# Performance work log

Hardware: AMD Instinct MI355X
Metric: run time of the kernel (lower is better)

## Reference

```python
import jax, jax.numpy as jnp
import numpy as np

B, S, D = 1, 2048, 2048
H, G = 32, 8            # n_heads, n_groups
HPG = H // G            # heads per group = 4
HD = D // H             # head_dim = 64


def setup_inputs() -> dict:
    key = jax.random.key(0)
    ks = jax.random.split(key, 5)
    w_scale = 0.02
    return {
        "x":  jax.random.normal(ks[0], (B, S, D), dtype=jnp.float32),
        "Wq": jax.random.normal(ks[1], (D, D), dtype=jnp.float32) * w_scale,
        "bq": jnp.zeros((D,), dtype=jnp.float32),
        "Wk": jax.random.normal(ks[2], (G * HD, D), dtype=jnp.float32) * w_scale,
        "bk": jnp.zeros((G * HD,), dtype=jnp.float32),
        "Wv": jax.random.normal(ks[3], (G * HD, D), dtype=jnp.float32) * w_scale,
        "bv": jnp.zeros((G * HD,), dtype=jnp.float32),
        "Wo": jax.random.normal(ks[4], (D, D), dtype=jnp.float32) * w_scale,
        "bo": jnp.zeros((D,), dtype=jnp.float32),
    }


def reference(x, Wq, bq, Wk, bk, Wv, bv, Wo, bo):
    b, n, _ = x.shape
    # projections (torch Linear: y = x @ W.T + b)
    q = x @ Wq.T + bq                              # [b, n, D]
    k = x @ Wk.T + bk                              # [b, n, G*HD]
    v = x @ Wv.T + bv                              # [b, n, G*HD]
    # q: [b, n, H, HD] -> [b, H, n, HD] -> split heads as (g h): [b, G, HPG, n, HD]
    q = q.reshape(b, n, H, HD).transpose(0, 2, 1, 3).reshape(b, G, HPG, n, HD)
    k = k.reshape(b, n, G, HD).transpose(0, 2, 1, 3)   # [b, G, n, HD]
    v = v.reshape(b, n, G, HD).transpose(0, 2, 1, 3)   # [b, G, n, HD]
    scale = 1.0 / jnp.sqrt(jnp.asarray(HD, dtype=q.dtype))
    attn_score = jnp.einsum('bghnd,bgsd->bghns', q, k) * scale
    attn_prob = jax.nn.softmax(attn_score, axis=-1)
    out = jnp.einsum('bghns,bgsd->bghnd', attn_prob, v)   # [b, G, HPG, n, HD]
    # faithful to original: rearrange 'b g h n d -> b n (h g d)' (h-major, g-minor)
    out = out.transpose(0, 3, 2, 1, 4).reshape(b, n, HPG * G * HD)
    return out @ Wo.T + bo
```

## Files before the change

### kernel.cpp

```cpp
#include <hip/hip_runtime.h>
#include <hip/hip_bf16.h>

constexpr int kS   = 2048;
constexpr int kD   = 2048;
constexpr int kG   = 8;
constexpr int kHD  = 64;
constexpr int kGHD = 512;
constexpr int kNQKV = kD + 2 * kGHD;

constexpr float kQScale = 0.125f * 1.4426950408889634f;

typedef __attribute__((ext_vector_type(8)))  _Float16 f16x8;
typedef __attribute__((ext_vector_type(4)))  float    f32x4;
typedef __attribute__((ext_vector_type(16))) float    f32x16;
typedef __attribute__((ext_vector_type(4)))  unsigned int u32x4;

__device__ __forceinline__ ushort f2h(float x) {
    return __builtin_bit_cast(ushort, (_Float16)x);
}
__device__ __forceinline__ float fast_exp2(float x) {
    return __builtin_amdgcn_exp2f(x);
}
__device__ __forceinline__ unsigned int pkrtz(float a, float b) {
    auto r = __builtin_amdgcn_cvt_pkrtz(a, b);
    return __builtin_bit_cast(unsigned int, r);
}

__global__ __launch_bounds__(256) void cvt_all(
    const float* __restrict__ x,  const float* __restrict__ Wq,
    const float* __restrict__ Wk, const float* __restrict__ Wv,
    const float* __restrict__ Wo, const float* __restrict__ bq,
    const float* __restrict__ bk, const float* __restrict__ bv,
    ushort* __restrict__ xf, ushort* __restrict__ wqkvf,
    ushort* __restrict__ wof, float* __restrict__ bqkv)
{
    constexpr size_t Nx  = (size_t)kS * kD;
    constexpr size_t NWq = (size_t)kD * kD;
    constexpr size_t NWk = (size_t)kGHD * kD;
    constexpr size_t e1 = Nx, e2 = e1 + NWq, e3 = e2 + NWk, e4 = e3 + NWk,
                     e5 = e4 + NWq;
    const size_t i = ((size_t)blockIdx.x * 256 + threadIdx.x) * 4;

    const float* src; ushort* dst; float scale = 1.f;
    if (i < e1)      { src = x  + i;        dst = xf + i; }
    else if (i < e2) { src = Wq + (i - e1); dst = wqkvf + (i - e1); scale = kQScale; }
    else if (i < e3) { src = Wk + (i - e2); dst = wqkvf + NWq + (i - e2); }
    else if (i < e4) { src = Wv + (i - e3); dst = wqkvf + NWq + NWk + (i - e3); }
    else if (i < e5) { src = Wo + (i - e4); dst = wof + (i - e4); }
    else {
        const size_t j = i - e5;
        #pragma unroll
        for (int u = 0; u < 4; ++u) {
            const size_t jj = j + u;
            if (jj < kD)              bqkv[jj] = bq[jj] * kQScale;
            else if (jj < kD + kGHD)  bqkv[jj] = bk[jj - kD];
            else if (jj < (size_t)kNQKV) bqkv[jj] = bv[jj - kD - kGHD];
        }
        return;
    }
    const float4 v = *(const float4*)src;
    ushort4 o;
    o.x = f2h(v.x * scale); o.y = f2h(v.y * scale);
    o.z = f2h(v.z * scale); o.w = f2h(v.w * scale);
    *(ushort4*)dst = o;
}

__device__ __forceinline__ int xcd_swizzle(int orig, int nwg) {
    const int cpx = nwg >> 3;
    return (orig & 7) * cpx + (orig >> 3);
}

#define GEMM_PRELUDE(Aptr, Bptr)                                              \
    const int bid  = xcd_swizzle(blockIdx.x, gridDim.x);                      \
    const int m0   = (bid / gridX) * 128;                                     \
    const int n0   = (bid % gridX) * 128;                                     \
    const int tid  = threadIdx.x;                                             \
    const int w    = tid >> 6;                                                \
    const int lane = tid & 63;                                                \
    const int kph  = w >> 2;                                                  \
    const int wm   = (w & 3) >> 1;                                            \
    const int wn   = w & 1;                                                   \
    const int fr   = lane & 15;                                               \
    const int kq   = lane >> 4;                                               \
    const int srow = w * 16 + (lane >> 3);                                    \
    const int sslot = ((lane & 7) ^ (lane >> 3)) * 8;                         \
    const ushort* gA = (Aptr) + (size_t)(m0 + srow) * K + sslot;              \
    const ushort* gB = (Bptr) + (size_t)(n0 + srow) * K + sslot;              \
    f32x4 acc[4][4];                                                          \
    _Pragma("unroll")                                                         \
    for (int mi = 0; mi < 4; ++mi)                                            \
        _Pragma("unroll")                                                     \
        for (int ni = 0; ni < 4; ++ni) {                                      \
            f32x4 z = {0.f, 0.f, 0.f, 0.f};                                   \
            acc[mi][ni] = z;                                                  \
        }

#define GEMM_STAGE(buf, k0)                                                   \
    do {                                                                      \
        _Pragma("unroll")                                                     \
        for (int j = 0; j < 2; ++j) {                                         \
            __builtin_amdgcn_global_load_lds(                                 \
                (const __attribute__((address_space(1))) void*)               \
                    (gA + (size_t)j * 8 * K + (k0)),                          \
                (__attribute__((address_space(3))) void*)                    \
                    &lds[buf][0][(w * 16 + j * 8) * 64],                      \
                16, 0, 0);                                                    \
            __builtin_amdgcn_global_load_lds(                                 \
                (const __attribute__((address_space(1))) void*)               \
                    (gB + (size_t)j * 8 * K + (k0)),                          \
                (__attribute__((address_space(3))) void*)                    \
                    &lds[buf][1][(w * 16 + j * 8) * 64],                      \
                16, 0, 0);                                                    \
        }                                                                     \
    } while (0)

#define GEMM_KLOOP                                                            \
    GEMM_STAGE(0, 0);                                                         \
    __syncthreads();                                                          \
    int cur = 0;                                                              \
    for (int k0 = 0; k0 < K; k0 += 64) {                                      \
        if (k0 + 64 < K) GEMM_STAGE(cur ^ 1, k0 + 64);                        \
        f16x8 af[4], bf[4];                                                   \
        _Pragma("unroll")                                                     \
        for (int f = 0; f < 4; ++f) {                                         \
            const int ra = wm * 64 + f * 16 + fr;                             \
            const int rb = wn * 64 + f * 16 + fr;                             \
            af[f] = *(const f16x8*)&lds[cur][0][ra * 64                       \
                        + (((kph * 4 + kq) ^ (ra & 7)) * 8)];                 \
            bf[f] = *(const f16x8*)&lds[cur][1][rb * 64                       \
                        + (((kph * 4 + kq) ^ (rb & 7)) * 8)];                 \
        }                                                                     \
        __builtin_amdgcn_s_setprio(1);                                        \
        _Pragma("unroll")                                                     \
        for (int mi = 0; mi < 4; ++mi)                                        \
            _Pragma("unroll")                                                 \
            for (int ni = 0; ni < 4; ++ni)                                    \
                acc[mi][ni] = __builtin_amdgcn_mfma_f32_16x16x32_f16(         \
                    af[mi], bf[ni], acc[mi][ni], 0, 0, 0);                    \
        __builtin_amdgcn_s_setprio(0);                                        \
        __syncthreads();                                                      \
        cur ^= 1;                                                             \
    }

#define GEMM_MERGE                                                            \
    float* mlds = (float*)&lds[0][0][0];                                      \
    if (w >= 4) {                                                             \
        _Pragma("unroll")                                                     \
        for (int c = 0; c < 16; ++c)                                          \
            *(f32x4*)&mlds[(w - 4) * 4096 + c * 256 + lane * 4]               \
                = acc[c >> 2][c & 3];                                         \
    }                                                                         \
    __syncthreads();                                                          \
    if (w < 4) {                                                              \
        _Pragma("unroll")                                                     \
        for (int c = 0; c < 16; ++c) {                                        \
            const f32x4 part = *(const f32x4*)&mlds[w * 4096 + c * 256        \
                                                    + lane * 4];              \
            acc[c >> 2][c & 3] += part;                                       \
        }                                                                     \
    }

__global__ __launch_bounds__(512, 4) void gemm_qkv(
    const ushort* __restrict__ Af, const ushort* __restrict__ Bf,
    const float* __restrict__ bias,
    ushort* __restrict__ qb16, ushort* __restrict__ kb16, ushort* __restrict__ vt16,
    int K, int gridX)
{
    __shared__ ushort lds[2][2][128 * 64];

    GEMM_PRELUDE(Af, Bf)
    GEMM_KLOOP
    GEMM_MERGE

    if (w < 4) {
        const int seg = (n0 < kD) ? 0 : (n0 < kD + kGHD) ? 1 : 2;
        #pragma unroll
        for (int ni = 0; ni < 4; ++ni) {
            const int ncol = n0 + wn * 64 + ni * 16 + fr;
            const float bv = bias[ncol];
            #pragma unroll
            for (int mi = 0; mi < 4; ++mi) {
                #pragma unroll
                for (int i = 0; i < 4; ++i) {
                    const int row = m0 + wm * 64 + mi * 16 + kq * 4 + i;
                    const ushort u = f2h(acc[mi][ni][i] + bv);
                    if (seg == 0)      qb16[(size_t)row * kD   + ncol]              = u;
                    else if (seg == 1) kb16[(size_t)row * kGHD + (ncol - kD)]       = u;
                    else               vt16[(size_t)(ncol - kD - kGHD) * kS + row]  = u;
                }
            }
        }
    }
}

__global__ __launch_bounds__(512, 4) void gemm_o(
    const ushort* __restrict__ Af, const ushort* __restrict__ Bf,
    const float* __restrict__ bias, float* __restrict__ C, int K, int N, int gridX)
{
    __shared__ ushort lds[2][2][128 * 64];

    GEMM_PRELUDE(Af, Bf)
    GEMM_KLOOP
    GEMM_MERGE

    if (w < 4) {
        #pragma unroll
        for (int ni = 0; ni < 4; ++ni) {
            const int ncol = n0 + wn * 64 + ni * 16 + fr;
            const float bv = bias[ncol];
            #pragma unroll
            for (int mi = 0; mi < 4; ++mi)
                #pragma unroll
                for (int i = 0; i < 4; ++i) {
                    const int row = m0 + wm * 64 + mi * 16 + kq * 4 + i;
                    C[(size_t)row * N + ncol] = acc[mi][ni][i] + bv;
                }
        }
    }
}

__global__ __launch_bounds__(512, 4) void gqa_attn_mfma(
    const ushort* __restrict__ qb,
    const ushort* __restrict__ kb,
    const ushort* __restrict__ vt,
    ushort* __restrict__ oh)
{
    __shared__ ushort Kt[2][2][64 * 64];
    __shared__ ushort Vt[2][2][64 * 64];

    const int g    = blockIdx.y;
    const int q0   = blockIdx.x * 32;
    const int tid  = threadIdx.x;
    const int w    = tid >> 6;
    const int lane = tid & 63;
    const int hw   = w & 3;
    const int half = w >> 2;
    const int ql   = lane & 31;
    const int hi   = lane >> 5;
    const int h    = g * 4 + hw;
    const int tbase = half * (kS / 2);

    const int r0 = hw * 16 + (lane >> 3);
    const int ss = (lane & 7) ^ (r0 & 7);

#define ATTN_STAGE(buf, t)                                                         \
    do {                                                                           \
        __builtin_amdgcn_global_load_lds(                                          \
            (const __attribute__((address_space(1))) void*)                       \
                (kb + (size_t)(tbase + (t) + r0) * kGHD + g * kHD + ss * 8),       \
            (__attribute__((address_space(3))) void*)(&Kt[half][buf][(hw * 16) * 64]), \
            16, 0, 0);                                                             \
        __builtin_amdgcn_global_load_lds(                                          \
            (const __attribute__((address_space(1))) void*)                       \
                (kb + (size_t)(tbase + (t) + r0 + 8) * kGHD + g * kHD + ss * 8),   \
            (__attribute__((address_space(3))) void*)(&Kt[half][buf][(hw * 16 + 8) * 64]), \
            16, 0, 0);                                                             \
        __builtin_amdgcn_global_load_lds(                                          \
            (const __attribute__((address_space(1))) void*)                       \
                (vt + (size_t)(g * kHD + r0) * kS + tbase + (t) + ss * 8),         \
            (__attribute__((address_space(3))) void*)(&Vt[half][buf][(hw * 16) * 64]), \
            16, 0, 0);                                                             \
        __builtin_amdgcn_global_load_lds(                                          \
            (const __attribute__((address_space(1))) void*)                       \
                (vt + (size_t)(g * kHD + r0 + 8) * kS + tbase + (t) + ss * 8),     \
            (__attribute__((address_space(3))) void*)(&Vt[half][buf][(hw * 16 + 8) * 64]), \
            16, 0, 0);                                                             \
    } while (0)

    ATTN_STAGE(0, 0);

    f16x8 qf[4];
    #pragma unroll
    for (int ks = 0; ks < 4; ++ks)
        qf[ks] = *(const f16x8*)&qb[(size_t)(q0 + ql) * kD + h * kHD + ks * 16 + hi * 8];

    float mrow = -1e30f, lrow = 0.f;
    f32x16 oacc[2];
    #pragma unroll
    for (int db = 0; db < 2; ++db)
        #pragma unroll
        for (int r = 0; r < 16; ++r) oacc[db][r] = 0.f;

    int cur = 0;
    for (int t = 0; t < kS / 2; t += 64) {
        __syncthreads();

        if (t + 64 < kS / 2) ATTN_STAGE(cur ^ 1, t + 64);

        f32x16 sc[2];
        #pragma unroll
        for (int kb2 = 0; kb2 < 2; ++kb2)
            #pragma unroll
            for (int r = 0; r < 16; ++r) sc[kb2][r] = 0.f;

        {
            f16x8 kf[2][4];
            #pragma unroll
            for (int kb2 = 0; kb2 < 2; ++kb2)
                #pragma unroll
                for (int ks = 0; ks < 4; ++ks)
                    kf[kb2][ks] = *(const f16x8*)&Kt[half][cur][(kb2 * 32 + ql) * 64
                                       + (((2 * ks + hi) ^ (ql & 7)) * 8)];
            __builtin_amdgcn_s_setprio(1);
            #pragma unroll
            for (int ks = 0; ks < 4; ++ks) {
                sc[0] = __builtin_amdgcn_mfma_f32_32x32x16_f16(kf[0][ks], qf[ks], sc[0], 0, 0, 0);
                sc[1] = __builtin_amdgcn_mfma_f32_32x32x16_f16(kf[1][ks], qf[ks], sc[1], 0, 0, 0);
            }
            __builtin_amdgcn_s_setprio(0);
        }

        float mt = sc[0][0];
        #pragma unroll
        for (int kb2 = 0; kb2 < 2; ++kb2)
            #pragma unroll
            for (int r = 0; r < 16; ++r) mt = fmaxf(mt, sc[kb2][r]);
        mt = fmaxf(mt, __shfl_xor(mt, 32));

        if (__any(mt > mrow + 11.5f)) {
            const float mnew = (mt > mrow + 11.5f) ? mt : mrow;
            const float c = fast_exp2(mrow - mnew);
            lrow *= c;
            mrow = mnew;
            #pragma unroll
            for (int db = 0; db < 2; ++db)
                #pragma unroll
                for (int r = 0; r < 16; ++r) oacc[db][r] *= c;
        }

        float ps = 0.f;
        #pragma unroll
        for (int kb2 = 0; kb2 < 2; ++kb2)
            #pragma unroll
            for (int r = 0; r < 16; ++r) {
                const float p = fast_exp2(sc[kb2][r] - mrow);
                sc[kb2][r] = p;
                ps += p;
            }
        ps += __shfl_xor(ps, 32);
        lrow += ps;

        {
            f16x8 pf[2][2];
            #pragma unroll
            for (int kb2 = 0; kb2 < 2; ++kb2)
                #pragma unroll
                for (int ks = 0; ks < 2; ++ks) {
                    unsigned int a0 = pkrtz(sc[kb2][8 * ks + 0], sc[kb2][8 * ks + 1]);
                    unsigned int a1 = pkrtz(sc[kb2][8 * ks + 2], sc[kb2][8 * ks + 3]);
                    unsigned int b0 = pkrtz(sc[kb2][8 * ks + 4], sc[kb2][8 * ks + 5]);
                    unsigned int b1 = pkrtz(sc[kb2][8 * ks + 6], sc[kb2][8 * ks + 7]);
                    asm volatile("v_permlane32_swap_b32 %0, %1" : "+v"(a0), "+v"(b0));
                    asm volatile("v_permlane32_swap_b32 %0, %1" : "+v"(a1), "+v"(b1));
                    const u32x4 pu = {a0, a1, b0, b1};
                    pf[kb2][ks] = __builtin_bit_cast(f16x8, pu);
                }
            f16x8 vf[2][2][2];
            #pragma unroll
            for (int kb2 = 0; kb2 < 2; ++kb2)
                #pragma unroll
                for (int ks = 0; ks < 2; ++ks)
                    #pragma unroll
                    for (int db = 0; db < 2; ++db)
                        vf[kb2][ks][db] = *(const f16x8*)&Vt[half][cur][(db * 32 + ql) * 64
                                             + (((4 * kb2 + 2 * ks + hi) ^ (ql & 7)) * 8)];
            __builtin_amdgcn_s_setprio(1);
            #pragma unroll
            for (int kb2 = 0; kb2 < 2; ++kb2)
                #pragma unroll
                for (int ks = 0; ks < 2; ++ks)
                    #pragma unroll
                    for (int db = 0; db < 2; ++db)
                        oacc[db] = __builtin_amdgcn_mfma_f32_32x32x16_f16(
                            vf[kb2][ks][db], pf[kb2][ks], oacc[db], 0, 0, 0);
            __builtin_amdgcn_s_setprio(0);
        }
        cur ^= 1;
    }
#undef ATTN_STAGE

    __syncthreads();
    float* ox  = (float*)(&Kt[0][0][0]);
    float* mlx = (float*)(&Vt[0][0][0]);
    const int idx = hw * 64 + lane;

    if (half == 1) {
        #pragma unroll
        for (int db = 0; db < 2; ++db)
            #pragma unroll
            for (int r = 0; r < 16; ++r)
                ox[(db * 16 + r) * 256 + idx] = oacc[db][r];
        mlx[idx]       = mrow;
        mlx[256 + idx] = lrow;
    }
    __syncthreads();

    if (half == 0) {
        const float m2 = mlx[idx];
        const float l2 = mlx[256 + idx];
        const float mm = fmaxf(mrow, m2);
        const float c1 = fast_exp2(mrow - mm);
        const float c2 = fast_exp2(m2 - mm);
        const float inv = 1.f / (lrow * c1 + l2 * c2);
        const size_t rowbase = (size_t)(q0 + ql) * kD + hw * kGHD + g * kHD;
        #pragma unroll
        for (int db = 0; db < 2; ++db) {
            #pragma unroll
            for (int rr = 0; rr < 4; ++rr) {
                ushort4 o4;
                o4.x = f2h((oacc[db][rr * 4 + 0] * c1 + ox[(db * 16 + rr * 4 + 0) * 256 + idx] * c2) * inv);
                o4.y = f2h((oacc[db][rr * 4 + 1] * c1 + ox[(db * 16 + rr * 4 + 1) * 256 + idx] * c2) * inv);
                o4.z = f2h((oacc[db][rr * 4 + 2] * c1 + ox[(db * 16 + rr * 4 + 2) * 256 + idx] * c2) * inv);
                o4.w = f2h((oacc[db][rr * 4 + 3] * c1 + ox[(db * 16 + rr * 4 + 3) * 256 + idx] * c2) * inv);
                *(ushort4*)&oh[rowbase + db * 32 + rr * 8 + hi * 4] = o4;
            }
        }
    }
}

extern "C" void kernel_launch(void* const* d_in, const int* in_sizes, int n_in,
                              void* d_out, int out_size, void* d_ws, size_t ws_size,
                              hipStream_t stream)
{
    const float* x  = (const float*)d_in[0];
    const float* Wq = (const float*)d_in[1];
    const float* bq = (const float*)d_in[2];
    const float* Wk = (const float*)d_in[3];
    const float* bk = (const float*)d_in[4];
    const float* Wv = (const float*)d_in[5];
    const float* bv = (const float*)d_in[6];
    const float* Wo = (const float*)d_in[7];
    const float* bo = (const float*)d_in[8];
    float* out = (float*)d_out;

    char* p = (char*)d_ws;
    ushort* xf    = (ushort*)p; p += (size_t)kS * kD * 2;
    ushort* wqkvf = (ushort*)p; p += (size_t)kNQKV * kD * 2;
    ushort* wof   = (ushort*)p; p += (size_t)kD * kD * 2;
    float*  bqkv  = (float*)p;  p += 16384;
    ushort* qb16  = (ushort*)p; p += (size_t)kS * kD * 2;
    ushort* kb16  = (ushort*)p; p += (size_t)kS * kGHD * 2;
    ushort* vt16  = (ushort*)p; p += (size_t)kGHD * kS * 2;
    ushort* aoh   = (ushort*)p;

    constexpr size_t kCvtElems = (size_t)kS * kD + 2 * (size_t)kD * kD
                               + 2 * (size_t)kGHD * kD + kNQKV;
    cvt_all<<<(kCvtElems + 1023) / 1024, 256, 0, stream>>>(
        x, Wq, Wk, Wv, Wo, bq, bk, bv, xf, wqkvf, wof, bqkv);

    gemm_qkv<<<(kNQKV / 128) * (kS / 128), 512, 0, stream>>>(
        xf, wqkvf, bqkv, qb16, kb16, vt16, kD, kNQKV / 128);

    gqa_attn_mfma<<<dim3(kS / 32, kG), 512, 0, stream>>>(qb16, kb16, vt16, aoh);

    gemm_o<<<(kD / 128) * (kS / 128), 512, 0, stream>>>(
        aoh, wof, bo, out, kD, kD, kD / 128);
}
```

Measured before the change: 134.7 us.

## Double GEMM K-tile to 128 and split K four ways across 16 waves

The QKV and output-projection GEMMs now use 1024-thread blocks: 16 waves, each a 4-way K-split of the 128x128 output tile. Each K step stages 128 columns of A and B, with every wave loading 16 rows of one matrix through a swizzled global-to-LDS path. A two-stage LDS reduction then merges the four partial accumulators. The aim is to halve the number of K iterations and barriers and raise MFMA work per sync. In exchange the LDS footprint doubles to 128KB, so probably only one block fits per CU, and the epilogue adds extra reduction barriers.

New measurement: 149.4 us. 1.11x slower.

```diff
diff --git a/kernel.cpp b/kernel.cpp
--- a/kernel.cpp
+++ b/kernel.cpp
@@ -75,17 +75,20 @@
     const int m0   = (bid / gridX) * 128;                                     \
     const int n0   = (bid % gridX) * 128;                                     \
     const int tid  = threadIdx.x;                                             \
-    const int w    = tid >> 6;                                                \
+    const int w    = tid >> 6;                                     \
     const int lane = tid & 63;                                                \
-    const int kph  = w >> 2;                                                  \
-    const int wm   = (w & 3) >> 1;                                            \
-    const int wn   = w & 1;                                                   \
+    const int kph  = w >> 2;                                \
+    const int sub  = w & 3;                                \
+    const int wm   = sub >> 1;                                                \
+    const int wn   = sub & 1;                                                 \
     const int fr   = lane & 15;                                               \
-    const int kq   = lane >> 4;                                               \
-    const int srow = w * 16 + (lane >> 3);                                    \
-    const int sslot = ((lane & 7) ^ (lane >> 3)) * 8;                         \
-    const ushort* gA = (Aptr) + (size_t)(m0 + srow) * K + sslot;              \
-    const ushort* gB = (Bptr) + (size_t)(n0 + srow) * K + sslot;              \
+    const int kq   = lane >> 4;                                     \
+    const int smat   = w >> 3;                    \
+    const int srbase = (w & 7) * 16;                    \
+    const int srsub  = lane >> 4;                 \
+    const int sslot  = lane & 15;              \
+    const ushort* gS = smat ? (Bptr) + (size_t)(n0 + srbase) * K              \
+                            : (Aptr) + (size_t)(m0 + srbase) * K;             \
     f32x4 acc[4][4];                                                          \
     _Pragma("unroll")                                                         \
     for (int mi = 0; mi < 4; ++mi)                                            \
@@ -98,18 +101,14 @@
 #define GEMM_STAGE(buf, k0)                                                   \
     do {                                                                      \
         _Pragma("unroll")                                                     \
-        for (int j = 0; j < 2; ++j) {                                         \
+        for (int j = 0; j < 4; ++j) {                                         \
+            const int rr = j * 4 + srsub;             \
+            const int s  = sslot ^ (rr & 7);         \
             __builtin_amdgcn_global_load_lds(                                 \
                 (const __attribute__((address_space(1))) void*)               \
-                    (gA + (size_t)j * 8 * K + (k0)),                          \
+                    (gS + (size_t)rr * K + (k0) + s * 8),                     \
                 (__attribute__((address_space(3))) void*)                    \
-                    &lds[buf][0][(w * 16 + j * 8) * 64],                      \
-                16, 0, 0);                                                    \
-            __builtin_amdgcn_global_load_lds(                                 \
-                (const __attribute__((address_space(1))) void*)               \
-                    (gB + (size_t)j * 8 * K + (k0)),                          \
-                (__attribute__((address_space(3))) void*)                    \
-                    &lds[buf][1][(w * 16 + j * 8) * 64],                      \
+                    &lds[buf][smat][(srbase + j * 4) * 128],                  \
                 16, 0, 0);                                                    \
         }                                                                     \
     } while (0)
@@ -118,16 +117,16 @@
     GEMM_STAGE(0, 0);                                                         \
     __syncthreads();                                                          \
     int cur = 0;                                                              \
-    for (int k0 = 0; k0 < K; k0 += 64) {                                      \
-        if (k0 + 64 < K) GEMM_STAGE(cur ^ 1, k0 + 64);                        \
+    for (int k0 = 0; k0 < K; k0 += 128) {                                     \
+        if (k0 + 128 < K) GEMM_STAGE(cur ^ 1, k0 + 128);                      \
         f16x8 af[4], bf[4];                                                   \
         _Pragma("unroll")                                                     \
         for (int f = 0; f < 4; ++f) {                                         \
             const int ra = wm * 64 + f * 16 + fr;                             \
             const int rb = wn * 64 + f * 16 + fr;                             \
-            af[f] = *(const f16x8*)&lds[cur][0][ra * 64                       \
+            af[f] = *(const f16x8*)&lds[cur][0][ra * 128                      \
                         + (((kph * 4 + kq) ^ (ra & 7)) * 8)];                 \
-            bf[f] = *(const f16x8*)&lds[cur][1][rb * 64                       \
+            bf[f] = *(const f16x8*)&lds[cur][1][rb * 128                      \
                         + (((kph * 4 + kq) ^ (rb & 7)) * 8)];                 \
         }                                                                     \
         __builtin_amdgcn_s_setprio(1);                                        \
@@ -144,35 +143,49 @@
 
 #define GEMM_MERGE                                                            \
     float* mlds = (float*)&lds[0][0][0];                                      \
-    if (w >= 4) {                                                             \
+    if (kph & 1) {                                                            \
+        const int d = (kph >> 1) * 4 + sub;                                   \
         _Pragma("unroll")                                                     \
         for (int c = 0; c < 16; ++c)                                          \
-            *(f32x4*)&mlds[(w - 4) * 4096 + c * 256 + lane * 4]               \
-                = acc[c >> 2][c & 3];                                         \
+            *(f32x4*)&mlds[d * 4096 + c * 256 + lane * 4] = acc[c >> 2][c & 3]; \
     }                                                                         \
     __syncthreads();                                                          \
-    if (w < 4) {                                                              \
+    if (!(kph & 1)) {                                                         \
+        const int d = (kph >> 1) * 4 + sub;                                   \
         _Pragma("unroll")                                                     \
         for (int c = 0; c < 16; ++c) {                                        \
-            const f32x4 part = *(const f32x4*)&mlds[w * 4096 + c * 256        \
-                                                    + lane * 4];              \
+            const f32x4 part = *(const f32x4*)&mlds[d * 4096 + c * 256 + lane * 4]; \
             acc[c >> 2][c & 3] += part;                                       \
         }                                                                     \
-    }
-
-__global__ __launch_bounds__(512, 4) void gemm_qkv(
+    }                                                                         \
+    __syncthreads();                                                          \
+    if (kph == 2) {                                                           \
+        _Pragma("unroll")                                                     \
+        for (int c = 0; c < 16; ++c)                                          \
+            *(f32x4*)&mlds[sub * 4096 + c * 256 + lane * 4] = acc[c >> 2][c & 3]; \
+    }                                                                         \
+    __syncthreads();                                                          \
+    if (kph == 0) {                                                           \
+        _Pragma("unroll")                                                     \
+        for (int c = 0; c < 16; ++c) {                                        \
+            const f32x4 part = *(const f32x4*)&mlds[sub * 4096 + c * 256 + lane * 4]; \
+            acc[c >> 2][c & 3] += part;                                       \
+        }                                                                     \
+    }
+
+__global__ __launch_bounds__(1024, 4) void gemm_qkv(
     const ushort* __restrict__ Af, const ushort* __restrict__ Bf,
     const float* __restrict__ bias,
     ushort* __restrict__ qb16, ushort* __restrict__ kb16, ushort* __restrict__ vt16,
     int K, int gridX)
 {
-    __shared__ ushort lds[2][2][128 * 64];
+    __shared__ ushort lds[2][2][128 * 128];
 
     GEMM_PRELUDE(Af, Bf)
     GEMM_KLOOP
     GEMM_MERGE
 
-    if (w < 4) {
+    if (kph == 0) {
         const int seg = (n0 < kD) ? 0 : (n0 < kD + kGHD) ? 1 : 2;
         #pragma unroll
         for (int ni = 0; ni < 4; ++ni) {
@@ -193,17 +206,17 @@
     }
 }
 
-__global__ __launch_bounds__(512, 4) void gemm_o(
+__global__ __launch_bounds__(1024, 4) void gemm_o(
     const ushort* __restrict__ Af, const ushort* __restrict__ Bf,
     const float* __restrict__ bias, float* __restrict__ C, int K, int N, int gridX)
 {
-    __shared__ ushort lds[2][2][128 * 64];
+    __shared__ ushort lds[2][2][128 * 128];
 
     GEMM_PRELUDE(Af, Bf)
     GEMM_KLOOP
     GEMM_MERGE
 
-    if (w < 4) {
+    if (kph == 0) {
         #pragma unroll
         for (int ni = 0; ni < 4; ++ni) {
             const int ncol = n0 + wn * 64 + ni * 16 + fr;
@@ -448,11 +461,11 @@
     cvt_all<<<(kCvtElems + 1023) / 1024, 256, 0, stream>>>(
         x, Wq, Wk, Wv, Wo, bq, bk, bv, xf, wqkvf, wof, bqkv);
 
-    gemm_qkv<<<(kNQKV / 128) * (kS / 128), 512, 0, stream>>>(
+    gemm_qkv<<<(kNQKV / 128) * (kS / 128), 1024, 0, stream>>>(
         xf, wqkvf, bqkv, qb16, kb16, vt16, kD, kNQKV / 128);
 
     gqa_attn_mfma<<<dim3(kS / 32, kG), 512, 0, stream>>>(qb16, kb16, vt16, aoh);
 
-    gemm_o<<<(kD / 128) * (kS / 128), 512, 0, stream>>>(
+    gemm_o<<<(kD / 128) * (kS / 128), 1024, 0, stream>>>(
         aoh, wof, bo, out, kD, kD, kD / 128);
 }
```
